# Kernel tuning notes

Hardware: AMD Instinct MI355X
Metric: run time of the kernel (lower is better)

Reference implementation:

```python
import jax, jax.numpy as jnp
import numpy as np

B, N, C, H, OUT = 4, 1024, 1024, 16, 1024
HEAD_DIM_INIT = C // H          # 64, used for scale per __init__
SCALE = HEAD_DIM_INIT ** -0.5
HD = 2 * C // H                 # 128, actual per-head dim after the reshape


def setup_inputs() -> dict:
    key = jax.random.key(0)
    k0, k1, k2, k3 = jax.random.split(key, 4)
    return {
        "x": jax.random.normal(k0, (B, N, C), jnp.float32),
        "context": jax.random.normal(k1, (B, N, C), jnp.float32),
        "w_qkv": jax.random.normal(k2, (3 * C, C), jnp.float32) / np.sqrt(C).astype(np.float32),
        "w_proj": jax.random.normal(k3, (OUT, C), jnp.float32) / np.sqrt(C).astype(np.float32),
        "b_proj": jnp.zeros((OUT,), jnp.float32),
    }


def reference(x, context, w_qkv, w_proj, b_proj):
    b, n, c = x.shape
    hd = 2 * c // H
    xc = jnp.concatenate([x, context], axis=1)                 # [B, 2N, C]
    qkv = jnp.einsum('bsc,dc->bsd', xc, w_qkv)                 # [B, 2N, 3C]
    # faithful to torch: reshape(B, N, 3, H, 2C/H) then permute(2,0,3,1,4)
    qkv = qkv.reshape(b, n, 3, H, hd).transpose(2, 0, 3, 1, 4)  # [3, B, H, N, HD]
    q, k, v = qkv[0], qkv[1], qkv[2]
    attn = jax.nn.softmax(jnp.einsum('bhqd,bhkd->bhqk', q, k) * SCALE, axis=-1)  # [B,H,N,N]
    o = jnp.einsum('bhqk,bhkd->bhqd', attn, v)                 # [B, H, N, HD]
    o = o.transpose(0, 2, 1, 3).reshape(b, 2 * n, c)           # [B, 2N, C]
    out = jnp.einsum('bsc,oc->bso', o, w_proj) + b_proj        # [B, 2N, OUT]
    return out, attn
```

## Files before the change

### kernel.cpp

```cpp
#include <hip/hip_runtime.h>
#include <stdint.h>

typedef short bf16x8 __attribute__((ext_vector_type(8)));
typedef short s16x4 __attribute__((ext_vector_type(4)));
typedef unsigned short us8 __attribute__((ext_vector_type(8)));
typedef float f32x4 __attribute__((ext_vector_type(4)));
typedef unsigned short u16;
typedef unsigned int u32;

__device__ __forceinline__ u16 f2bf(float f) {
    u32 u = __float_as_uint(f);
    return (u16)((u + 0x7FFFu + ((u >> 16) & 1u)) >> 16);
}
__device__ __forceinline__ float bf2f(u16 h) { return __uint_as_float(((u32)h) << 16); }

__device__ __forceinline__ u32 cvtpk(float lo, float hi) {
    u32 r;
    asm("v_cvt_pk_bf16_f32 %0, %1, %2" : "=v"(r) : "v"(lo), "v"(hi));
    return r;
}

typedef __attribute__((address_space(3))) unsigned int lds_uint;
typedef const __attribute__((address_space(1))) unsigned int glb_uint;
__device__ __forceinline__ void gld16(const void* g, void* l) {
    __builtin_amdgcn_global_load_lds((glb_uint*)g, (lds_uint*)l, 16, 0, 0);
}

#define VWAIT(n) asm volatile("s_waitcnt vmcnt(" #n ") lgkmcnt(0)" ::: "memory")
#define LWAIT    asm volatile("s_waitcnt lgkmcnt(0)" ::: "memory")
#define BARRIER  do { __builtin_amdgcn_s_barrier(); __builtin_amdgcn_sched_barrier(0); } while (0)


__device__ __forceinline__ void gld_p128x32(const u16* __restrict__ g, int64_t stride,
                                            u16* lds, int w, int lane) {
#pragma unroll
    for (int i = 0; i < 2; ++i) {
        const int grp = w * 2 + i;
        const int row = grp * 16 + (lane >> 2);
        const int sl = (lane & 3) ^ ((row >> 1) & 3);
        gld16(g + (int64_t)row * stride + (sl << 3), &lds[grp * 512]);
    }
}
__device__ __forceinline__ int idx128x32(int row, int gk) {
    return row * 32 + ((gk ^ ((row >> 1) & 3)) << 3);
}

__device__ __forceinline__ void gld_t32x128(const u16* __restrict__ g, int64_t stride,
                                            u16* lds, int w, int lane) {
#pragma unroll
    for (int i = 0; i < 2; ++i) {
        const int gg = w * 2 + i;
        const int row = gg * 4 + (lane >> 4);
        const int gs = (lane & 15) ^ (row & 7);
        gld16(g + (int64_t)row * stride + (gs << 3), &lds[gg * 512]);
    }
}
__device__ __forceinline__ void gld_t64x128(const u16* __restrict__ g, int64_t stride,
                                            u16* lds, int w, int lane) {
#pragma unroll
    for (int i = 0; i < 4; ++i) {
        const int gg = w * 4 + i;
        const int row = gg * 4 + (lane >> 4);
        const int gs = (lane & 15) ^ (row & 7);
        gld16(g + (int64_t)row * stride + (gs << 3), &lds[gg * 512]);
    }
}
__device__ __forceinline__ int idxT(int row, int gk) {
    return row * 128 + ((gk ^ (row & 7)) << 3);
}

__device__ __forceinline__ void gld_v128x64(const u16* __restrict__ g, int64_t stride,
                                            u16* lds, int w, int lane) {
#pragma unroll
    for (int i = 0; i < 4; ++i) {
        const int seg = w * 4 + i;
        const int row = seg * 8 + (lane >> 3);
        const int gs = (lane & 7) ^ (row & 7);
        gld16(g + (int64_t)row * stride + (gs << 3), &lds[seg * 512]);
    }
}
__device__ __forceinline__ int idxV(int row, int g3) {
    return row * 64 + ((g3 ^ (row & 7)) << 3);
}

__device__ __forceinline__ void mfma_step1(const u16* LA, const u16* LB,
                                           int wrow, int wcol, int lane,
                                           f32x4 acc[4][4]) {
    const int rl = lane & 15, gk = lane >> 4;
    bf16x8 a[4], bv[4];
#pragma unroll
    for (int i = 0; i < 4; ++i) {
        a[i]  = *reinterpret_cast<const bf16x8*>(&LA[idx128x32(wrow + i * 16 + rl, gk)]);
        bv[i] = *reinterpret_cast<const bf16x8*>(&LB[idx128x32(wcol + i * 16 + rl, gk)]);
    }
#pragma unroll
    for (int m = 0; m < 4; ++m)
#pragma unroll
        for (int n = 0; n < 4; ++n)
            acc[m][n] = __builtin_amdgcn_mfma_f32_16x16x32_bf16(a[m], bv[n], acc[m][n], 0, 0, 0);
}

__global__ void k0_all(const float* __restrict__ wqkv, const float* __restrict__ x,
                       const float* __restrict__ ctx, const float* __restrict__ wproj,
                       u16* __restrict__ Wh, u16* __restrict__ Xh,
                       u16* __restrict__ Phw) {
    const int gid = blockIdx.x;
    const float* src; u16* dst; int mode; int lg;
    if (gid < 1536)      { src = wqkv;  dst = Wh;  mode = 0; lg = gid; }
    else if (gid < 3584) { src = x;     dst = Xh;  mode = 1; lg = gid - 1536; }
    else if (gid < 5632) { src = ctx;   dst = Xh;  mode = 2; lg = gid - 3584; }
    else                 { src = wproj; dst = Phw; mode = 0; lg = gid - 5632; }
    const int64_t base = ((int64_t)lg * 256 + threadIdx.x) * 8;
    const int row = (int)(base >> 10), col = (int)(base & 1023);
    int orow = row;
    if (mode == 1) orow = row + ((row >> 10) << 10);
    else if (mode == 2) orow = row + (((row >> 10) + 1) << 10);
    const float4* sp = reinterpret_cast<const float4*>(src + base);
    float4 a = sp[0], b = sp[1];
    float v[8] = {a.x, a.y, a.z, a.w, b.x, b.y, b.z, b.w};
    us8 hh;
#pragma unroll
    for (int j = 0; j < 8; ++j) hh[j] = f2bf(v[j]);
    *reinterpret_cast<us8*>(&dst[(int64_t)orow * 1024 + col]) = hh;
}

__global__ __launch_bounds__(512, 1) void k1_qkv(const u16* __restrict__ Xh,
                                                 const u16* __restrict__ Wh,
                                                 u16* __restrict__ Qh) {
    __shared__ u16 L[4][2][8192];
    const int tid = threadIdx.x, lane = tid & 63;
    const int w = tid >> 6, wm = w >> 2, wn = w & 3;
    const int rl = lane & 15, gk = lane >> 4, r4 = gk << 2;
    const int n0 = blockIdx.x << 8, m0 = blockIdx.y << 8;
    const u16* Ab = Xh + (int64_t)m0 * 1024;
    const u16* Bb = Wh + (int64_t)n0 * 1024;
    const int srow0 = tid >> 3, scol = tid & 7;
    f32x4 acc[2][4][2][2] = {};
    bf16x8 afr[4][2];

#define STAGE1(X, KT) do { if ((KT) < 16) {                                      \
    const u16* _b = (((X) < 2) ? (Ab + (int64_t)((X) * 128) * 1024)              \
                               : (Bb + (int64_t)(((X) - 2) * 128) * 1024))       \
                    + (KT) * 64;                                                 \
    u16* _l = &L[(X)][(KT) & 1][0];                                              \
    _Pragma("unroll") for (int _j = 0; _j < 2; ++_j) {                           \
        const int _r = _j * 64 + srow0;                                          \
        const int _g = scol ^ (_r & 7);                                          \
        gld16(_b + (int64_t)_r * 1024 + _g * 8, &_l[_r * 64 + scol * 8]);        \
    } } } while (0)

#define RDF(X, PAR, ROW, KHGK)                                                   \
    (*reinterpret_cast<const bf16x8*>(                                           \
        &L[(X)][(PAR)][(ROW) * 64 + (((KHGK) ^ ((ROW) & 7)) << 3)]))

#define PHASE(QM, QN, PAR, STX, STKT) do {                                       \
    STAGE1(STX, STKT);                                                           \
    VWAIT(6);                                                                    \
    __builtin_amdgcn_s_barrier(); __builtin_amdgcn_sched_barrier(0);             \
    if ((QN) == 0) {                                                             \
        _Pragma("unroll") for (int _mf = 0; _mf < 4; ++_mf) {                    \
            afr[_mf][0] = RDF(QM, PAR, wm * 64 + _mf * 16 + rl, gk);             \
            afr[_mf][1] = RDF(QM, PAR, wm * 64 + _mf * 16 + rl, 4 + gk);         \
        } }                                                                      \
    bf16x8 _b00 = RDF(2 + (QN), PAR, wn * 32 + rl, gk);                          \
    bf16x8 _b01 = RDF(2 + (QN), PAR, wn * 32 + rl, 4 + gk);                      \
    bf16x8 _b10 = RDF(2 + (QN), PAR, wn * 32 + 16 + rl, gk);                     \
    bf16x8 _b11 = RDF(2 + (QN), PAR, wn * 32 + 16 + rl, 4 + gk);                 \
    LWAIT; __builtin_amdgcn_sched_barrier(0);                                    \
    __builtin_amdgcn_s_setprio(1);                                               \
    _Pragma("unroll") for (int _mf = 0; _mf < 4; ++_mf) {                        \
        acc[QM][_mf][QN][0] = __builtin_amdgcn_mfma_f32_16x16x32_bf16(           \
            afr[_mf][0], _b00, acc[QM][_mf][QN][0], 0, 0, 0);                    \
        acc[QM][_mf][QN][0] = __builtin_amdgcn_mfma_f32_16x16x32_bf16(           \
            afr[_mf][1], _b01, acc[QM][_mf][QN][0], 0, 0, 0);                    \
        acc[QM][_mf][QN][1] = __builtin_amdgcn_mfma_f32_16x16x32_bf16(           \
            afr[_mf][0], _b10, acc[QM][_mf][QN][1], 0, 0, 0);                    \
        acc[QM][_mf][QN][1] = __builtin_amdgcn_mfma_f32_16x16x32_bf16(           \
            afr[_mf][1], _b11, acc[QM][_mf][QN][1], 0, 0, 0);                    \
    }                                                                            \
    __builtin_amdgcn_s_setprio(0);                                               \
    __builtin_amdgcn_s_barrier(); __builtin_amdgcn_sched_barrier(0);             \
} while (0)

    STAGE1(0, 0); STAGE1(2, 0); STAGE1(1, 0); STAGE1(3, 0); STAGE1(0, 1); STAGE1(2, 1);
    for (int i = 0; i < 8; ++i) {
        const int t = 2 * i;
        PHASE(0, 0, 0, 1, t + 1);
        PHASE(0, 1, 0, 3, t + 1);
        PHASE(1, 0, 0, 0, t + 2);
        PHASE(1, 1, 0, 2, t + 2);
        PHASE(0, 0, 1, 1, t + 2);
        PHASE(0, 1, 1, 3, t + 2);
        PHASE(1, 0, 1, 0, t + 3);
        PHASE(1, 1, 1, 2, t + 3);
    }
#undef PHASE
#undef RDF
#undef STAGE1
#pragma unroll
    for (int qm = 0; qm < 2; ++qm)
#pragma unroll
        for (int mf = 0; mf < 4; ++mf)
#pragma unroll
            for (int qn = 0; qn < 2; ++qn)
#pragma unroll
                for (int nf = 0; nf < 2; ++nf)
#pragma unroll
                    for (int j = 0; j < 4; ++j) {
                        const int row = m0 + qm * 128 + wm * 64 + mf * 16 + r4 + j;
                        const int col = n0 + qn * 128 + wn * 32 + nf * 16 + rl;
                        Qh[(int64_t)row * 3072 + col] = f2bf(acc[qm][mf][qn][nf][j]);
                    }
}

__global__ __launch_bounds__(256, 2) void k0v_vt(const u16* __restrict__ Qh,
                                                 u16* __restrict__ Vt) {
    __shared__ u16 T[128][144];
    const int tid = threadIdx.x;
    const int z = blockIdx.y, b = z >> 4, h = z & 15;
    const int kt = blockIdx.x;
    const int c0v = (h < 8) ? (1024 + h * 128) : (2048 + (h - 8) * 128);
    const u16* Vbase = Qh + ((int64_t)b * 2048 + 1) * 3072 + c0v;
    const int row = tid >> 1, e0 = (tid & 1) << 6;
    const u16* src = Vbase + (int64_t)(kt * 128 + row) * 6144 + e0;
#pragma unroll
    for (int i = 0; i < 8; ++i) {
        us8 v = *reinterpret_cast<const us8*>(src + i * 8);
#pragma unroll
        for (int j = 0; j < 8; ++j) T[e0 + i * 8 + j][row] = v[j];
    }
    __syncthreads();
    const int e = tid >> 1, k0 = (tid & 1) << 6;
    u16* dst = Vt + ((int64_t)z << 17) + (int64_t)e * 1024 + kt * 128 + k0;
#pragma unroll
    for (int i = 0; i < 8; ++i)
        *reinterpret_cast<us8*>(dst + i * 8) = *reinterpret_cast<const us8*>(&T[e][k0 + i * 8]);
}

__global__ __launch_bounds__(256, 2) void k23_fused(const u16* __restrict__ Qh,
                                                    const u16* __restrict__ Vt,
                                                    float* __restrict__ attn,
                                                    u16* __restrict__ Obf) {
    __shared__ u16 LQ[4096];
    __shared__ u16 LKV[3][8192];
    __shared__ u16 Ph[32 * 72];
    __shared__ float pS[4][32];
    __shared__ float rowInv[32];
    const int tid = threadIdx.x, lane = tid & 63, w = tid >> 6;
    const u32 wgid = blockIdx.x;
    const int xcd = wgid & 7, t0 = wgid >> 3;
    const int mt = t0 & 31, z = ((t0 >> 5) << 3) + xcd;
    const int b = z >> 4, h = z & 15;
    const int m0 = mt << 5;
    const u16* Qbase = Qh + ((int64_t)b * 2048 + 2 * m0) * 3072 + h * 128;
    const int pk  = (h < 8) ? 0 : 1;
    const int c0k = (h < 8) ? (2048 + h * 128) : ((h - 8) * 128);
    const u16* Kbase = Qh + ((int64_t)b * 2048 + pk) * 3072 + c0k;
    const u16* Vtz = Vt + ((int64_t)z << 17);
    float* attnZ = attn + ((int64_t)z << 20) + (int64_t)m0 * 1024;
    const int rl = lane & 15, gk = lane >> 4;
    const int r4 = gk << 2;
    const int sm = w & 1, sn = w >> 1;
    gld_t32x128(Qbase, 6144, LQ, w, lane);
    gld_t64x128(Kbase,             6144, LKV[0], w, lane);
    gld_t64x128(Kbase + 64 * 6144, 6144, LKV[1], w, lane);
    u32 pk0[32], pk1[32];
    float ssum0 = 0.f, ssum1 = 0.f;
#pragma unroll
    for (int t = 0; t < 16; ++t) {
        if (t == 15) { VWAIT(0); } else { VWAIT(4); }
        BARRIER;
        if (t < 14)
            gld_t64x128(Kbase + (int64_t)(t + 2) * 64 * 6144, 6144, LKV[(t + 2) % 3], w, lane);
        f32x4 s0 = {}, s1 = {};
#pragma unroll
        for (int ks = 0; ks < 4; ++ks) {
            bf16x8 kf = *reinterpret_cast<const bf16x8*>(&LKV[t % 3][idxT(w * 16 + rl, ks * 4 + gk)]);
            bf16x8 q0 = *reinterpret_cast<const bf16x8*>(&LQ[idxT(rl, ks * 4 + gk)]);
            bf16x8 q1 = *reinterpret_cast<const bf16x8*>(&LQ[idxT(16 + rl, ks * 4 + gk)]);
            s0 = __builtin_amdgcn_mfma_f32_16x16x32_bf16(kf, q0, s0, 0, 0, 0);
            s1 = __builtin_amdgcn_mfma_f32_16x16x32_bf16(kf, q1, s1, 0, 0, 0);
        }
        float p0[4], p1[4];
#pragma unroll
        for (int j = 0; j < 4; ++j) {
            p0[j] = __expf(s0[j] * 0.125f); ssum0 += p0[j];
            p1[j] = __expf(s1[j] * 0.125f); ssum1 += p1[j];
        }
        pk0[2 * t]     = cvtpk(p0[0], p0[1]);
        pk1[2 * t]     = cvtpk(p0[2], p0[3]);
        pk0[2 * t + 1] = cvtpk(p1[0], p1[1]);
        pk1[2 * t + 1] = cvtpk(p1[2], p1[3]);
    }
    ssum0 += __shfl_xor(ssum0, 16); ssum0 += __shfl_xor(ssum0, 32);
    ssum1 += __shfl_xor(ssum1, 16); ssum1 += __shfl_xor(ssum1, 32);
    if (lane < 16) { pS[w][lane] = ssum0; pS[w][16 + lane] = ssum1; }
    LWAIT; BARRIER;
    gld_v128x64(Vtz,      1024, LKV[0], w, lane);
    gld_v128x64(Vtz + 64, 1024, LKV[1], w, lane);
    if (tid < 32)
        rowInv[tid] = 1.0f / (pS[0][tid] + pS[1][tid] + pS[2][tid] + pS[3][tid]);
    LWAIT; BARRIER;
    const float Iq0 = rowInv[rl], Iq1 = rowInv[16 + rl];
    float IqO[4];
#pragma unroll
    for (int j = 0; j < 4; ++j) IqO[j] = rowInv[sm * 16 + r4 + j];
    f32x4 po[4] = {};
#pragma unroll
    for (int t = 0; t < 16; ++t) {
        if (t == 0)       { VWAIT(4); }
        else if (t == 15) { VWAIT(2); }
        else              { VWAIT(6); }
        BARRIER;
        if (t < 14)
            gld_v128x64(Vtz + (t + 2) * 64, 1024, LKV[(t + 2) % 3], w, lane);
        const u32 a0 = pk0[2 * t], a1 = pk1[2 * t];
        const u32 b0 = pk0[2 * t + 1], b1 = pk1[2 * t + 1];
        *reinterpret_cast<uint2*>(&Ph[rl * 72 + w * 16 + r4])        = make_uint2(a0, a1);
        *reinterpret_cast<uint2*>(&Ph[(16 + rl) * 72 + w * 16 + r4]) = make_uint2(b0, b1);
        *reinterpret_cast<float4*>(&attnZ[(int64_t)rl * 1024 + t * 64 + w * 16 + r4])
            = make_float4(__uint_as_float(a0 << 16) * Iq0,
                          __uint_as_float(a0 & 0xFFFF0000u) * Iq0,
                          __uint_as_float(a1 << 16) * Iq0,
                          __uint_as_float(a1 & 0xFFFF0000u) * Iq0);
        *reinterpret_cast<float4*>(&attnZ[(int64_t)(16 + rl) * 1024 + t * 64 + w * 16 + r4])
            = make_float4(__uint_as_float(b0 << 16) * Iq1,
                          __uint_as_float(b0 & 0xFFFF0000u) * Iq1,
                          __uint_as_float(b1 << 16) * Iq1,
                          __uint_as_float(b1 & 0xFFFF0000u) * Iq1);
        LWAIT; BARRIER;
        bf16x8 pa0 = *reinterpret_cast<const bf16x8*>(&Ph[(sm * 16 + rl) * 72 + gk * 8]);
        bf16x8 pa1 = *reinterpret_cast<const bf16x8*>(&Ph[(sm * 16 + rl) * 72 + 32 + gk * 8]);
#pragma unroll
        for (int n = 0; n < 4; ++n) {
            bf16x8 bv0 = *reinterpret_cast<const bf16x8*>(&LKV[t % 3][idxV(sn * 64 + n * 16 + rl, gk)]);
            bf16x8 bv1 = *reinterpret_cast<const bf16x8*>(&LKV[t % 3][idxV(sn * 64 + n * 16 + rl, 4 + gk)]);
            po[n] = __builtin_amdgcn_mfma_f32_16x16x32_bf16(pa0, bv0, po[n], 0, 0, 0);
            po[n] = __builtin_amdgcn_mfma_f32_16x16x32_bf16(pa1, bv1, po[n], 0, 0, 0);
        }
    }
    const int poh = h >> 3, cb2 = (h & 7) << 7;
#pragma unroll
    for (int n = 0; n < 4; ++n)
#pragma unroll
        for (int j = 0; j < 4; ++j) {
            const int qrow = m0 + sm * 16 + r4 + j;
            Obf[((int64_t)b * 2048 + 2 * qrow + poh) * 1024
                + cb2 + sn * 64 + n * 16 + rl] = f2bf(po[n][j] * IqO[j]);
        }
}

__global__ __launch_bounds__(256, 2) void k4_out(const u16* __restrict__ Obf,
                                                 const u16* __restrict__ Phw,
                                                 const float* __restrict__ bias,
                                                 float* __restrict__ out) {
    __shared__ u16 LA[4096], LB[4096];
    const int tid = threadIdx.x, lane = tid & 63, w = tid >> 6;
    const int wrow = (w >> 1) << 6, wcol = (w & 1) << 6;
    const int n0 = blockIdx.x << 7, m0 = blockIdx.y << 7;
    const u16* Ab = Obf + (int64_t)m0 * 1024;
    const u16* Bb = Phw + (int64_t)n0 * 1024;
    f32x4 acc[4][4] = {};
    for (int kb = 0; kb < 32; ++kb) {
        gld_p128x32(Ab + kb * 32, 1024, LA, w, lane);
        gld_p128x32(Bb + kb * 32, 1024, LB, w, lane);
        __syncthreads();
        mfma_step1(LA, LB, wrow, wcol, lane, acc);
        __syncthreads();
    }
    const int r4 = (lane >> 4) << 2, cc = lane & 15;
#pragma unroll
    for (int m = 0; m < 4; ++m)
#pragma unroll
        for (int n = 0; n < 4; ++n)
#pragma unroll
            for (int j = 0; j < 4; ++j)
                out[(int64_t)(m0 + wrow + m * 16 + r4 + j) * 1024
                    + (n0 + wcol + n * 16 + cc)]
                    = acc[m][n][j] + bias[n0 + wcol + n * 16 + cc];
}

extern "C" void kernel_launch(void* const* d_in, const int* in_sizes, int n_in,
                              void* d_out, int out_size, void* d_ws, size_t ws_size,
                              hipStream_t stream) {
    const float* x     = (const float*)d_in[0];
    const float* ctx   = (const float*)d_in[1];
    const float* wqkv  = (const float*)d_in[2];
    const float* wproj = (const float*)d_in[3];
    const float* bias  = (const float*)d_in[4];
    float* out  = (float*)d_out;
    float* attn = out + 8388608;

    u16* Qh  = (u16*)d_ws;
    u16* Vt  = Qh + 25165824;
    u16* Wh  = Vt + 8388608;
    u16* Phw = Wh + 3145728;
    u16* Obf = Phw + 1048576;

    u16* Xh = (u16*)attn;

    k0_all   <<<dim3(6144),   256, 0, stream>>>(wqkv, x, ctx, wproj, Wh, Xh, Phw);
    k1_qkv   <<<dim3(12, 32), 512, 0, stream>>>(Xh, Wh, Qh);
    k0v_vt   <<<dim3(8, 64),  256, 0, stream>>>(Qh, Vt);
    k23_fused<<<dim3(2048),   256, 0, stream>>>(Qh, Vt, attn, Obf);
    k4_out   <<<dim3(8, 64),  256, 0, stream>>>(Obf, Phw, bias, out);
}
```

Baseline: 243.0 us.

## Generalize pipelined 8-phase GEMM to 256x128 tiles and reuse for output projection

```diff
diff --git a/kernel.cpp b/kernel.cpp
--- a/kernel.cpp
+++ b/kernel.cpp
@@ -81,23 +81,6 @@
 }
 __device__ __forceinline__ int idxV(int row, int g3) {
     return row * 64 + ((g3 ^ (row & 7)) << 3);
-}
-
-__device__ __forceinline__ void mfma_step1(const u16* LA, const u16* LB,
-                                           int wrow, int wcol, int lane,
-                                           f32x4 acc[4][4]) {
-    const int rl = lane & 15, gk = lane >> 4;
-    bf16x8 a[4], bv[4];
-#pragma unroll
-    for (int i = 0; i < 4; ++i) {
-        a[i]  = *reinterpret_cast<const bf16x8*>(&LA[idx128x32(wrow + i * 16 + rl, gk)]);
-        bv[i] = *reinterpret_cast<const bf16x8*>(&LB[idx128x32(wcol + i * 16 + rl, gk)]);
-    }
-#pragma unroll
-    for (int m = 0; m < 4; ++m)
-#pragma unroll
-        for (int n = 0; n < 4; ++n)
-            acc[m][n] = __builtin_amdgcn_mfma_f32_16x16x32_bf16(a[m], bv[n], acc[m][n], 0, 0, 0);
 }
 
 __global__ void k0_all(const float* __restrict__ wqkv, const float* __restrict__ x,
@@ -124,25 +107,27 @@
     *reinterpret_cast<us8*>(&dst[(int64_t)orow * 1024 + col]) = hh;
 }
 
-__global__ __launch_bounds__(512, 1) void k1_qkv(const u16* __restrict__ Xh,
-                                                 const u16* __restrict__ Wh,
-                                                 u16* __restrict__ Qh) {
-    __shared__ u16 L[4][2][8192];
+template<bool ISK4>
+__global__ __launch_bounds__(512, 1) void gemm8p(const u16* __restrict__ Ap,
+                                                 const u16* __restrict__ Bp,
+                                                 const float* __restrict__ bias,
+                                                 u16* __restrict__ outh,
+                                                 float* __restrict__ outf) {
+    __shared__ u16 L[3][2][8192];
     const int tid = threadIdx.x, lane = tid & 63;
     const int w = tid >> 6, wm = w >> 2, wn = w & 3;
     const int rl = lane & 15, gk = lane >> 4, r4 = gk << 2;
-    const int n0 = blockIdx.x << 8, m0 = blockIdx.y << 8;
-    const u16* Ab = Xh + (int64_t)m0 * 1024;
-    const u16* Bb = Wh + (int64_t)n0 * 1024;
+    const int n0 = blockIdx.x << 7, m0 = blockIdx.y << 8;
+    const u16* Ab = Ap + (int64_t)m0 * 1024;
+    const u16* Bb = Bp + (int64_t)n0 * 1024;
     const int srow0 = tid >> 3, scol = tid & 7;
-    f32x4 acc[2][4][2][2] = {};
+    f32x4 acc[2][4][2] = {};
     bf16x8 afr[4][2];
 
-#define STAGE1(X, KT) do { if ((KT) < 16) {                                      \
-    const u16* _b = (((X) < 2) ? (Ab + (int64_t)((X) * 128) * 1024)              \
-                               : (Bb + (int64_t)(((X) - 2) * 128) * 1024))       \
+#define STAGE1(X, KT) do { if ((X) >= 0 && (KT) < 16) {                          \
+    const u16* _b = (((X) < 2) ? (Ab + (int64_t)((X) * 128) * 1024) : Bb)        \
                     + (KT) * 64;                                                 \
-    u16* _l = &L[(X)][(KT) & 1][0];                                              \
+    u16* _l = &L[((X) < 0) ? 0 : (X)][(KT) & 1][0];                              \
     _Pragma("unroll") for (int _j = 0; _j < 2; ++_j) {                           \
         const int _r = _j * 64 + srow0;                                          \
         const int _g = scol ^ (_r & 7);                                          \
@@ -153,46 +138,40 @@
     (*reinterpret_cast<const bf16x8*>(                                           \
         &L[(X)][(PAR)][(ROW) * 64 + (((KHGK) ^ ((ROW) & 7)) << 3)]))
 
-#define PHASE(QM, QN, PAR, STX, STKT) do {                                       \
+#define PHASE(QM, QN, PAR, STX, STKT, WMODE) do {                                \
     STAGE1(STX, STKT);                                                           \
-    VWAIT(6);                                                                    \
+    if ((WMODE) == 1) { VWAIT(4); } else if ((WMODE) == 2) { VWAIT(0); }         \
     __builtin_amdgcn_s_barrier(); __builtin_amdgcn_sched_barrier(0);             \
     if ((QN) == 0) {                                                             \
         _Pragma("unroll") for (int _mf = 0; _mf < 4; ++_mf) {                    \
             afr[_mf][0] = RDF(QM, PAR, wm * 64 + _mf * 16 + rl, gk);             \
             afr[_mf][1] = RDF(QM, PAR, wm * 64 + _mf * 16 + rl, 4 + gk);         \
         } }                                                                      \
-    bf16x8 _b00 = RDF(2 + (QN), PAR, wn * 32 + rl, gk);                          \
-    bf16x8 _b01 = RDF(2 + (QN), PAR, wn * 32 + rl, 4 + gk);                      \
-    bf16x8 _b10 = RDF(2 + (QN), PAR, wn * 32 + 16 + rl, gk);                     \
-    bf16x8 _b11 = RDF(2 + (QN), PAR, wn * 32 + 16 + rl, 4 + gk);                 \
+    bf16x8 _b0 = RDF(2, PAR, (QN) * 64 + wn * 16 + rl, gk);                      \
+    bf16x8 _b1 = RDF(2, PAR, (QN) * 64 + wn * 16 + rl, 4 + gk);                  \
     LWAIT; __builtin_amdgcn_sched_barrier(0);                                    \
     __builtin_amdgcn_s_setprio(1);                                               \
     _Pragma("unroll") for (int _mf = 0; _mf < 4; ++_mf) {                        \
-        acc[QM][_mf][QN][0] = __builtin_amdgcn_mfma_f32_16x16x32_bf16(           \
-            afr[_mf][0], _b00, acc[QM][_mf][QN][0], 0, 0, 0);                    \
-        acc[QM][_mf][QN][0] = __builtin_amdgcn_mfma_f32_16x16x32_bf16(           \
-            afr[_mf][1], _b01, acc[QM][_mf][QN][0], 0, 0, 0);                    \
-        acc[QM][_mf][QN][1] = __builtin_amdgcn_mfma_f32_16x16x32_bf16(           \
-            afr[_mf][0], _b10, acc[QM][_mf][QN][1], 0, 0, 0);                    \
-        acc[QM][_mf][QN][1] = __builtin_amdgcn_mfma_f32_16x16x32_bf16(           \
-            afr[_mf][1], _b11, acc[QM][_mf][QN][1], 0, 0, 0);                    \
+        acc[QM][_mf][QN] = __builtin_amdgcn_mfma_f32_16x16x32_bf16(              \
+            afr[_mf][0], _b0, acc[QM][_mf][QN], 0, 0, 0);                        \
+        acc[QM][_mf][QN] = __builtin_amdgcn_mfma_f32_16x16x32_bf16(              \
+            afr[_mf][1], _b1, acc[QM][_mf][QN], 0, 0, 0);                        \
     }                                                                            \
     __builtin_amdgcn_s_setprio(0);                                               \
     __builtin_amdgcn_s_barrier(); __builtin_amdgcn_sched_barrier(0);             \
 } while (0)
 
-    STAGE1(0, 0); STAGE1(2, 0); STAGE1(1, 0); STAGE1(3, 0); STAGE1(0, 1); STAGE1(2, 1);
+    STAGE1(0, 0); STAGE1(1, 0); STAGE1(2, 0); STAGE1(0, 1);
     for (int i = 0; i < 8; ++i) {
         const int t = 2 * i;
-        PHASE(0, 0, 0, 1, t + 1);
-        PHASE(0, 1, 0, 3, t + 1);
-        PHASE(1, 0, 0, 0, t + 2);
-        PHASE(1, 1, 0, 2, t + 2);
-        PHASE(0, 0, 1, 1, t + 2);
-        PHASE(0, 1, 1, 3, t + 2);
-        PHASE(1, 0, 1, 0, t + 3);
-        PHASE(1, 1, 1, 2, t + 3);
+        PHASE(0, 0, 0, 1, t + 1, 1);
+        PHASE(0, 1, 0, 2, t + 1, 0);
+        PHASE(1, 0, 0, 0, t + 2, 0);
+        PHASE(1, 1, 0, -1, 0, 0);
+        PHASE(0, 0, 1, 1, t + 2, (i == 7) ? 2 : 1);
+        PHASE(0, 1, 1, 2, t + 2, 0);
+        PHASE(1, 0, 1, 0, t + 3, 0);
+        PHASE(1, 1, 1, -1, 0, 0);
     }
 #undef PHASE
 #undef RDF
@@ -204,13 +183,14 @@
 #pragma unroll
             for (int qn = 0; qn < 2; ++qn)
 #pragma unroll
-                for (int nf = 0; nf < 2; ++nf)
-#pragma unroll
-                    for (int j = 0; j < 4; ++j) {
-                        const int row = m0 + qm * 128 + wm * 64 + mf * 16 + r4 + j;
-                        const int col = n0 + qn * 128 + wn * 32 + nf * 16 + rl;
-                        Qh[(int64_t)row * 3072 + col] = f2bf(acc[qm][mf][qn][nf][j]);
-                    }
+                for (int j = 0; j < 4; ++j) {
+                    const int row = m0 + qm * 128 + wm * 64 + mf * 16 + r4 + j;
+                    const int col = n0 + qn * 64 + wn * 16 + rl;
+                    if (ISK4)
+                        outf[(int64_t)row * 1024 + col] = acc[qm][mf][qn][j] + bias[col];
+                    else
+                        outh[(int64_t)row * 3072 + col] = f2bf(acc[qm][mf][qn][j]);
+                }
 }
 
 __global__ __launch_bounds__(256, 2) void k0v_vt(const u16* __restrict__ Qh,
@@ -350,36 +330,6 @@
         }
 }
 
-__global__ __launch_bounds__(256, 2) void k4_out(const u16* __restrict__ Obf,
-                                                 const u16* __restrict__ Phw,
-                                                 const float* __restrict__ bias,
-                                                 float* __restrict__ out) {
-    __shared__ u16 LA[4096], LB[4096];
-    const int tid = threadIdx.x, lane = tid & 63, w = tid >> 6;
-    const int wrow = (w >> 1) << 6, wcol = (w & 1) << 6;
-    const int n0 = blockIdx.x << 7, m0 = blockIdx.y << 7;
-    const u16* Ab = Obf + (int64_t)m0 * 1024;
-    const u16* Bb = Phw + (int64_t)n0 * 1024;
-    f32x4 acc[4][4] = {};
-    for (int kb = 0; kb < 32; ++kb) {
-        gld_p128x32(Ab + kb * 32, 1024, LA, w, lane);
-        gld_p128x32(Bb + kb * 32, 1024, LB, w, lane);
-        __syncthreads();
-        mfma_step1(LA, LB, wrow, wcol, lane, acc);
-        __syncthreads();
-    }
-    const int r4 = (lane >> 4) << 2, cc = lane & 15;
-#pragma unroll
-    for (int m = 0; m < 4; ++m)
-#pragma unroll
-        for (int n = 0; n < 4; ++n)
-#pragma unroll
-            for (int j = 0; j < 4; ++j)
-                out[(int64_t)(m0 + wrow + m * 16 + r4 + j) * 1024
-                    + (n0 + wcol + n * 16 + cc)]
-                    = acc[m][n][j] + bias[n0 + wcol + n * 16 + cc];
-}
-
 extern "C" void kernel_launch(void* const* d_in, const int* in_sizes, int n_in,
                               void* d_out, int out_size, void* d_ws, size_t ws_size,
                               hipStream_t stream) {
@@ -399,9 +349,9 @@
 
     u16* Xh = (u16*)attn;
 
-    k0_all   <<<dim3(6144),   256, 0, stream>>>(wqkv, x, ctx, wproj, Wh, Xh, Phw);
-    k1_qkv   <<<dim3(12, 32), 512, 0, stream>>>(Xh, Wh, Qh);
-    k0v_vt   <<<dim3(8, 64),  256, 0, stream>>>(Qh, Vt);
-    k23_fused<<<dim3(2048),   256, 0, stream>>>(Qh, Vt, attn, Obf);
-    k4_out   <<<dim3(8, 64),  256, 0, stream>>>(Obf, Phw, bias, out);
-}
+    k0_all        <<<dim3(6144),   256, 0, stream>>>(wqkv, x, ctx, wproj, Wh, Xh, Phw);
+    gemm8p<false> <<<dim3(24, 32), 512, 0, stream>>>(Xh, Wh, nullptr, Qh, nullptr);
+    k0v_vt        <<<dim3(8, 64),  256, 0, stream>>>(Qh, Vt);
+    k23_fused     <<<dim3(2048),   256, 0, stream>>>(Qh, Vt, attn, Obf);
+    gemm8p<true>  <<<dim3(8, 32),  512, 0, stream>>>(Obf, Phw, bias, nullptr, out);
+}
```

New measurement: 231.8 us. 4.6% less time.
